# Kernel tuning notes

Measured on AMD Instinct MI355X. Metric: run time of the kernel, lower is better.

Reference implementation:

```python
import jax, jax.numpy as jnp
import numpy as np

B, N, D, H, DFF, V, L, ASTHOP = 16, 512, 256, 8, 1024, 50000, 2, 2
NEG_INF = -1e9
LRELU_SLOPE = 0.2
LN_EPS = 1e-6


def positional_encoding(length, d):
    pos = np.arange(length)[:, None].astype(np.float32)
    i = np.arange(d)[None, :].astype(np.float32)
    angle = pos / np.power(10000.0, (2.0 * np.floor(i / 2.0)) / d)
    pe = np.zeros((length, d), dtype=np.float32)
    pe[:, 0::2] = np.sin(angle[:, 0::2])
    pe[:, 1::2] = np.cos(angle[:, 1::2])
    return jnp.asarray(pe[None])  # [1, length, d]


def layer_norm(x, g, b):
    mu = jnp.mean(x, axis=-1, keepdims=True)
    var = jnp.mean((x - mu) ** 2, axis=-1, keepdims=True)
    return (x - mu) * jax.lax.rsqrt(var + LN_EPS) * g + b


def setup_inputs() -> dict:
    key = jax.random.key(0)
    ks = jax.random.split(key, 16)
    s = 0.02
    f32 = jnp.float32
    return {
        "node_input": jax.random.randint(ks[0], (B, N), 0, V, dtype=jnp.int32),
        "edge_input": jax.random.randint(ks[1], (B, N, N), 0, 2, dtype=jnp.int32),
        "mha_mask": jnp.zeros((B, 1, 1, N), jnp.int32),
        "training": 0,
        "embed": jax.random.normal(ks[2], (V, D), f32) * s,
        "Wg": jax.random.normal(ks[3], (D, D), f32) * s,
        "a1": jax.random.normal(ks[4], (D, 1), f32) * s,
        "a2": jax.random.normal(ks[5], (D, 1), f32) * s,
        "Wq": jax.random.normal(ks[6], (L, D, D), f32) * s,
        "bq": jnp.zeros((L, D), f32),
        "Wk": jax.random.normal(ks[7], (L, D, D), f32) * s,
        "bk": jnp.zeros((L, D), f32),
        "Wv": jax.random.normal(ks[8], (L, D, D), f32) * s,
        "bv": jnp.zeros((L, D), f32),
        "Wo": jax.random.normal(ks[9], (L, D, D), f32) * s,
        "bo": jnp.zeros((L, D), f32),
        "W1": jax.random.normal(ks[10], (L, D, DFF), f32) * s,
        "b1": jnp.zeros((L, DFF), f32),
        "W2": jax.random.normal(ks[11], (L, DFF, D), f32) * s,
        "b2": jnp.zeros((L, D), f32),
        "ln1_g": jnp.ones((L, D), f32),
        "ln1_b": jnp.zeros((L, D), f32),
        "ln2_g": jnp.ones((L, D), f32),
        "ln2_b": jnp.zeros((L, D), f32),
    }


def reference(node_input, edge_input, mha_mask, training, embed, Wg, a1, a2,
              Wq, bq, Wk, bk, Wv, bv, Wo, bo, W1, b1, W2, b2,
              ln1_g, ln1_b, ln2_g, ln2_b):
    del training  # inference: dropout is identity
    pe = positional_encoding(N, D)
    adj = edge_input > 0  # [B,N,N] bool

    x = embed[node_input]  # [B,N,D] embedding lookup
    # --- GAT message-passing hops (shared weights) ---
    for _ in range(ASTHOP):
        h = x @ Wg  # [B,N,D]
        # e_ij = LeakyReLU(a1.h_i + a2.h_j)
        e = jax.nn.leaky_relu(h @ a1 + jnp.swapaxes(h @ a2, 1, 2), LRELU_SLOPE)
        e = jnp.where(adj, e, NEG_INF)
        alpha = jax.nn.softmax(e, axis=-1)  # [B,N,N]
        x = jax.nn.elu(jnp.einsum('bij,bjd->bid', alpha, h))

    # --- scale + positional encoding ---
    x = x * jnp.sqrt(jnp.float32(D)) + pe[:, :N, :]

    # --- transformer encoder stack ---
    mask = mha_mask.astype(x.dtype)  # [B,1,1,N], 1 = pad
    dh = D // H
    attn = None
    for l in range(L):
        q = (x @ Wq[l] + bq[l]).reshape(B, N, H, dh).transpose(0, 2, 1, 3)
        k = (x @ Wk[l] + bk[l]).reshape(B, N, H, dh).transpose(0, 2, 1, 3)
        v = (x @ Wv[l] + bv[l]).reshape(B, N, H, dh).transpose(0, 2, 1, 3)
        scores = jnp.einsum('bhqd,bhkd->bhqk', q, k) / jnp.sqrt(jnp.float32(dh))
        scores = scores + mask * NEG_INF
        attn = jax.nn.softmax(scores, axis=-1)  # [B,H,N,N]
        o = jnp.einsum('bhqk,bhkd->bhqd', attn, v).transpose(0, 2, 1, 3).reshape(B, N, D)
        x = layer_norm(x + o @ Wo[l] + bo[l], ln1_g[l], ln1_b[l])
        f = jax.nn.relu(x @ W1[l] + b1[l]) @ W2[l] + b2[l]
        x = layer_norm(x + f, ln2_g[l], ln2_b[l])
    return (x, attn)
```

## Files before the change

kernel.cpp:

```cpp
#include <hip/hip_runtime.h>
#include <math.h>

#define B_    16
#define N_    512
#define D_    256
#define H_    8
#define DH_   32
#define DFF_  1024
#define L_    2
#define NEG_INF_ (-1e9f)
#define LRELU_ 0.2f

typedef __attribute__((ext_vector_type(8))) short bf8_t;
typedef __attribute__((ext_vector_type(8))) unsigned short us8;
typedef __attribute__((ext_vector_type(4))) float f4_t;

__device__ __forceinline__ unsigned short f2bf(float f) {
    union { float f; unsigned u; } v; v.f = f;
    unsigned r = v.u + 0x7FFF + ((v.u >> 16) & 1);
    return (unsigned short)(r >> 16);
}
__device__ __forceinline__ float bf2f(unsigned short h) {
    union { unsigned u; float f; } v; v.u = ((unsigned)h) << 16;
    return v.f;
}

__device__ __forceinline__ void gl_lds16(const void* g, void* l) {
    __builtin_amdgcn_global_load_lds(
        (const __attribute__((address_space(1))) unsigned int*)g,
        (__attribute__((address_space(3))) unsigned int*)l, 16, 0, 0);
}

template <int BM, int BN, int WROWS, int WCOLS>
__global__ __launch_bounds__(256) void mfma_gemm(
    const unsigned short* __restrict__ Ag, const unsigned short* __restrict__ Btg,
    const float* __restrict__ bias,
    float* __restrict__ Cfg, unsigned short* __restrict__ Chg, int trans,
    int K, int lda, int ldb, int ldc,
    int inner, long sAo, long sAi, long sBo, long sBi, long sCo, long sCi,
    float scale, int act)
{
    constexpr int TM = BM / WROWS, TN = BN / WCOLS;
    constexpr int MT = TM / 16, NT = TN / 16;

    int z  = blockIdx.z;
    int zo = z / inner;
    int zi = z - zo * inner;
    const unsigned short* Ab = Ag + (long)zo * sAo + (long)zi * sAi;
    const unsigned short* Bt = Btg + (long)zo * sBo + (long)zi * sBi;
    long co = (long)zo * sCo + (long)zi * sCi;

    int bm = blockIdx.y * BM;
    int bn = blockIdx.x * BN;
    int tid  = threadIdx.x;
    int lane = tid & 63;
    int w    = tid >> 6;
    int wr   = w / WCOLS, wc = w - wr * WCOLS;

    __shared__ unsigned short As[BM * 32];
    __shared__ unsigned short Bs[BN * 32];

    f4_t acc[MT][NT] = {};

    int lrow = lane & 15;
    int koff = (lane >> 4) * 8;

    for (int k0 = 0; k0 < K; k0 += 32) {
#pragma unroll
        for (int t = w; t < BM / 16; t += 4) {
            int s = t * 512 + lane * 8;
            int r = s >> 5, c = s & 31;
            gl_lds16(Ab + (long)(bm + r) * lda + k0 + c, &As[t * 512]);
        }
#pragma unroll
        for (int t = w; t < BN / 16; t += 4) {
            int s = t * 512 + lane * 8;
            int r = s >> 5, c = s & 31;
            gl_lds16(Bt + (long)(bn + r) * ldb + k0 + c, &Bs[t * 512]);
        }
        __syncthreads();

        bf8_t af[MT], bfr[NT];
#pragma unroll
        for (int mi = 0; mi < MT; mi++)
            af[mi] = *(const bf8_t*)&As[(wr * TM + mi * 16 + lrow) * 32 + koff];
#pragma unroll
        for (int ni = 0; ni < NT; ni++)
            bfr[ni] = *(const bf8_t*)&Bs[(wc * TN + ni * 16 + lrow) * 32 + koff];
#pragma unroll
        for (int mi = 0; mi < MT; mi++)
#pragma unroll
            for (int ni = 0; ni < NT; ni++)
                acc[mi][ni] = __builtin_amdgcn_mfma_f32_16x16x32_bf16(
                    af[mi], bfr[ni], acc[mi][ni], 0, 0, 0);
        __syncthreads();
    }

#pragma unroll
    for (int mi = 0; mi < MT; mi++) {
#pragma unroll
        for (int ni = 0; ni < NT; ni++) {
            int row0 = bm + wr * TM + mi * 16 + (lane >> 4) * 4;
            int col  = bn + wc * TN + ni * 16 + (lane & 15);
            float bv = bias ? bias[col] : 0.f;
            float vv[4];
#pragma unroll
            for (int r = 0; r < 4; r++) {
                float v = acc[mi][ni][r] * scale + bv;
                if (act == 1) v = fmaxf(v, 0.f);
                else if (act == 2) v = v > 0.f ? v : (__expf(v) - 1.f);
                vv[r] = v;
            }
            if (trans) {
                ushort4 u = make_ushort4(f2bf(vv[0]), f2bf(vv[1]), f2bf(vv[2]), f2bf(vv[3]));
                *(ushort4*)&Chg[co + (long)col * ldc + row0] = u;
            } else {
                if (Cfg) {
#pragma unroll
                    for (int r = 0; r < 4; r++)
                        Cfg[co + (long)(row0 + r) * ldc + col] = vv[r];
                }
                if (Chg) {
#pragma unroll
                    for (int r = 0; r < 4; r++)
                        Chg[co + (long)(row0 + r) * ldc + col] = f2bf(vv[r]);
                }
            }
        }
    }
}

template <bool WRITE_ATTN>
__global__ __launch_bounds__(256) void attn_fused(
    const unsigned short* __restrict__ QKV,
    const int* __restrict__ mask,
    float* __restrict__ attn_out,
    unsigned short* __restrict__ Ob)
{
    int bh = blockIdx.x;
    int b  = bh >> 3, h = bh & 7;
    int q0 = blockIdx.y * 64;
    int tid  = threadIdx.x;
    int lane = tid & 63, w = tid >> 6;
    int lrow = lane & 15, quad = lane >> 4;

    __shared__ unsigned short Ks[512 * 40];
    __shared__ unsigned short Vs[32 * 136];
    __shared__ float maskf[512];
    unsigned short* Ps = Ks;

    const long tokbase = (long)b * N_;

#pragma unroll
    for (int i = 0; i < 8; i++) {
        int idx = tid + i * 256;
        int row = idx >> 2, seg = idx & 3;
        us8 v = *(const us8*)&QKV[(tokbase + row) * 768 + 256 + h * 32 + seg * 8];
        *(us8*)&Ks[row * 40 + seg * 8] = v;
    }
    maskf[tid]       = (float)mask[b * N_ + tid] * NEG_INF_;
    maskf[tid + 256] = (float)mask[b * N_ + tid + 256] * NEG_INF_;

    bf8_t aq = *(const bf8_t*)&QKV[(tokbase + q0 + w * 16 + lrow) * 768 + h * 32 + quad * 8];
    __syncthreads();

    f4_t acc[32];
    f4_t zero = {0.f, 0.f, 0.f, 0.f};
#pragma unroll
    for (int ni = 0; ni < 32; ni++) {
        bf8_t bk = *(const bf8_t*)&Ks[(ni * 16 + lrow) * 40 + quad * 8];
        acc[ni] = __builtin_amdgcn_mfma_f32_16x16x32_bf16(aq, bk, zero, 0, 0, 0);
    }

    const float rscale = 0.17677669529663687f;
    float mr[4] = {-3e38f, -3e38f, -3e38f, -3e38f};
#pragma unroll
    for (int ni = 0; ni < 32; ni++) {
        float mk = maskf[ni * 16 + lrow];
#pragma unroll
        for (int r = 0; r < 4; r++) {
            float v = acc[ni][r] * rscale + mk;
            acc[ni][r] = v;
            mr[r] = fmaxf(mr[r], v);
        }
    }
#pragma unroll
    for (int r = 0; r < 4; r++) {
        mr[r] = fmaxf(mr[r], __shfl_xor(mr[r], 1));
        mr[r] = fmaxf(mr[r], __shfl_xor(mr[r], 2));
        mr[r] = fmaxf(mr[r], __shfl_xor(mr[r], 4));
        mr[r] = fmaxf(mr[r], __shfl_xor(mr[r], 8));
    }
    float sr[4] = {0.f, 0.f, 0.f, 0.f};
#pragma unroll
    for (int ni = 0; ni < 32; ni++) {
#pragma unroll
        for (int r = 0; r < 4; r++) {
            float p = __expf(acc[ni][r] - mr[r]);
            acc[ni][r] = p;
            sr[r] += p;
        }
    }
#pragma unroll
    for (int r = 0; r < 4; r++) {
        sr[r] += __shfl_xor(sr[r], 1);
        sr[r] += __shfl_xor(sr[r], 2);
        sr[r] += __shfl_xor(sr[r], 4);
        sr[r] += __shfl_xor(sr[r], 8);
        sr[r] = 1.f / sr[r];
    }
#pragma unroll
    for (int ni = 0; ni < 32; ni++)
#pragma unroll
        for (int r = 0; r < 4; r++)
            acc[ni][r] *= sr[r];

    if (WRITE_ATTN) {
#pragma unroll
        for (int ni = 0; ni < 32; ni++) {
#pragma unroll
            for (int r = 0; r < 4; r++)
                attn_out[((long)bh * N_ + q0 + w * 16 + quad * 4 + r) * N_ + ni * 16 + lrow]
                    = acc[ni][r];
        }
    }

    f4_t oacc[2] = {{0.f,0.f,0.f,0.f}, {0.f,0.f,0.f,0.f}};
    for (int c = 0; c < 4; c++) {
        __syncthreads();
        {
            int kk = tid >> 1, dseg = (tid & 1) * 16;
            const unsigned short* src =
                &QKV[(tokbase + c * 128 + kk) * 768 + 512 + h * 32 + dseg];
            us8 v0 = *(const us8*)src;
            us8 v1 = *(const us8*)(src + 8);
#pragma unroll
            for (int jj = 0; jj < 8; jj++) {
                Vs[(dseg + jj) * 136 + kk]     = v0[jj];
                Vs[(dseg + 8 + jj) * 136 + kk] = v1[jj];
            }
        }
#pragma unroll
        for (int ni = 0; ni < 8; ni++) {
            int nn = c * 8 + ni;
#pragma unroll
            for (int r = 0; r < 4; r++)
                Ps[w * 2176 + (quad * 4 + r) * 136 + ni * 16 + lrow] = f2bf(acc[nn][r]);
        }
        __syncthreads();
#pragma unroll
        for (int k8 = 0; k8 < 4; k8++) {
            bf8_t ap = *(const bf8_t*)&Ps[w * 2176 + lrow * 136 + k8 * 32 + quad * 8];
#pragma unroll
            for (int t = 0; t < 2; t++) {
                bf8_t bvf = *(const bf8_t*)&Vs[(t * 16 + lrow) * 136 + k8 * 32 + quad * 8];
                oacc[t] = __builtin_amdgcn_mfma_f32_16x16x32_bf16(ap, bvf, oacc[t], 0, 0, 0);
            }
        }
    }

#pragma unroll
    for (int t = 0; t < 2; t++)
#pragma unroll
        for (int r = 0; r < 4; r++)
            Ob[(tokbase + q0 + w * 16 + quad * 4 + r) * 256 + h * 32 + t * 16 + lrow]
                = f2bf(oacc[t][r]);
}

struct ConvJobs {
    const float* src[13];
    unsigned short* dst[13];
    int R[13];
    int C[13];
};

__global__ __launch_bounds__(256) void conv_transpose(ConvJobs j)
{
    int z = blockIdx.z;
    int R = j.R[z], C = j.C[z];
    int r0 = blockIdx.y * 64, c0 = blockIdx.x * 64;
    if (r0 >= R || c0 >= C) return;
    __shared__ float t[64][65];
    const float* src = j.src[z];
    unsigned short* dst = j.dst[z];
    int tx = threadIdx.x & 63, ty = threadIdx.x >> 6;
#pragma unroll
    for (int i = 0; i < 16; i++) {
        int r = ty + i * 4;
        t[r][tx] = src[(long)(r0 + r) * C + c0 + tx];
    }
    __syncthreads();
#pragma unroll
    for (int i = 0; i < 16; i++) {
        int c = ty + i * 4;
        dst[(long)(c0 + c) * R + r0 + tx] = f2bf(t[tx][c]);
    }
}

__global__ __launch_bounds__(256) void pack_bias(const float* __restrict__ bq,
                                                 const float* __restrict__ bk,
                                                 const float* __restrict__ bv,
                                                 float* __restrict__ bc)
{
    int i = blockIdx.x * 256 + threadIdx.x;
    int l = i / 768, c = i - l * 768;
    float v = (c < 256) ? bq[l * 256 + c]
            : (c < 512) ? bk[l * 256 + c - 256]
                        : bv[l * 256 + c - 512];
    bc[i] = v;
}

__global__ __launch_bounds__(64) void gather_embed(const int* __restrict__ idx,
                                                   const float* __restrict__ embed,
                                                   float* __restrict__ X,
                                                   unsigned short* __restrict__ Xb)
{
    int row = blockIdx.x;
    int id  = idx[row];
    float4 v = ((const float4*)(embed + (long)id * D_))[threadIdx.x];
    ((float4*)(X + (long)row * D_))[threadIdx.x] = v;
    ((ushort4*)(Xb + (long)row * D_))[threadIdx.x] =
        make_ushort4(f2bf(v.x), f2bf(v.y), f2bf(v.z), f2bf(v.w));
}

__global__ __launch_bounds__(256) void gat_s12T(const unsigned short* __restrict__ hT,
                                                const float* __restrict__ a1,
                                                const float* __restrict__ a2,
                                                float* __restrict__ s1,
                                                float* __restrict__ s2)
{
    int j = blockIdx.x * 256 + threadIdx.x;
    float d1 = 0.f, d2 = 0.f;
    for (int d = 0; d < D_; d++) {
        float hv = bf2f(hT[(long)d * (B_ * N_) + j]);
        d1 += hv * a1[d];
        d2 += hv * a2[d];
    }
    s1[j] = d1;
    s2[j] = d2;
}

__global__ __launch_bounds__(256) void gat_alpha(const float* __restrict__ s1,
                                                 const float* __restrict__ s2,
                                                 const int* __restrict__ edges,
                                                 unsigned short* __restrict__ alpha)
{
    int row = blockIdx.x;
    int b   = row >> 9;
    const int*   erow = edges + (long)row * N_;
    const float* s2b  = s2 + (long)b * N_;
    float si = s1[row];
    int t = threadIdx.x;

    float e  = si + s2b[t];
    e = e > 0.f ? e : LRELU_ * e;
    float v0 = (erow[t] > 0) ? e : NEG_INF_;
    float e2 = si + s2b[t + 256];
    e2 = e2 > 0.f ? e2 : LRELU_ * e2;
    float v1 = (erow[t + 256] > 0) ? e2 : NEG_INF_;

    __shared__ float redm[4], reds[4];
    float m = fmaxf(v0, v1);
    for (int off = 32; off; off >>= 1) m = fmaxf(m, __shfl_xor(m, off));
    if ((t & 63) == 0) redm[t >> 6] = m;
    __syncthreads();
    m = fmaxf(fmaxf(redm[0], redm[1]), fmaxf(redm[2], redm[3]));
    float x0 = __expf(v0 - m), x1 = __expf(v1 - m);
    float s = x0 + x1;
    for (int off = 32; off; off >>= 1) s += __shfl_xor(s, off);
    if ((t & 63) == 0) reds[t >> 6] = s;
    __syncthreads();
    s = reds[0] + reds[1] + reds[2] + reds[3];
    float inv = 1.f / s;
    alpha[(long)row * N_ + t]       = f2bf(x0 * inv);
    alpha[(long)row * N_ + t + 256] = f2bf(x1 * inv);
}

__global__ __launch_bounds__(64) void ln_add(const float* __restrict__ x,
                                             const float* __restrict__ tm,
                                             const float* __restrict__ g,
                                             const float* __restrict__ bta,
                                             float* __restrict__ out,
                                             unsigned short* __restrict__ outb)
{
    long row  = blockIdx.x;
    int  lane = threadIdx.x;
    float4 xv = ((const float4*)(x + row * D_))[lane];
    float4 tv = ((const float4*)(tm + row * D_))[lane];
    float4 v = make_float4(xv.x + tv.x, xv.y + tv.y, xv.z + tv.z, xv.w + tv.w);
    float s = v.x + v.y + v.z + v.w;
    for (int off = 32; off; off >>= 1) s += __shfl_xor(s, off);
    float mean = s * (1.f / D_);
    float4 d = make_float4(v.x - mean, v.y - mean, v.z - mean, v.w - mean);
    float sq = d.x * d.x + d.y * d.y + d.z * d.z + d.w * d.w;
    for (int off = 32; off; off >>= 1) sq += __shfl_xor(sq, off);
    float rs = rsqrtf(sq * (1.f / D_) + 1e-6f);
    float4 gv = ((const float4*)g)[lane];
    float4 bv = ((const float4*)bta)[lane];
    float4 o = make_float4(d.x * rs * gv.x + bv.x, d.y * rs * gv.y + bv.y,
                           d.z * rs * gv.z + bv.z, d.w * rs * gv.w + bv.w);
    ((float4*)(out + row * D_))[lane] = o;
    ((ushort4*)(outb + row * D_))[lane] =
        make_ushort4(f2bf(o.x), f2bf(o.y), f2bf(o.z), f2bf(o.w));
}

__global__ __launch_bounds__(256) void scale_pe(float* __restrict__ X,
                                                unsigned short* __restrict__ Xb)
{
    int row = blockIdx.x;
    int n = row & (N_ - 1);
    int d = threadIdx.x;
    float expo = (float)(d & ~1) * (1.0f / D_);
    float inv  = powf(10000.0f, -expo);
    float ang  = (float)n * inv;
    float pe   = (d & 1) ? cosf(ang) : sinf(ang);
    long idx = (long)row * D_ + d;
    float v = X[idx] * 16.0f + pe;
    X[idx]  = v;
    Xb[idx] = f2bf(v);
}

__global__ __launch_bounds__(256) void copy_f4(const float4* __restrict__ src,
                                               float4* __restrict__ dst, long n4)
{
    long i = (long)blockIdx.x * 256 + threadIdx.x;
    if (i < n4) dst[i] = src[i];
}

extern "C" void kernel_launch(void* const* d_in, const int* in_sizes, int n_in,
                              void* d_out, int out_size, void* d_ws, size_t ws_size,
                              hipStream_t stream)
{
    const int*   node  = (const int*)d_in[0];
    const int*   edge  = (const int*)d_in[1];
    const int*   mask  = (const int*)d_in[2];
    const float* embed = (const float*)d_in[4];
    const float* Wg    = (const float*)d_in[5];
    const float* a1    = (const float*)d_in[6];
    const float* a2    = (const float*)d_in[7];
    const float* Wq    = (const float*)d_in[8];
    const float* bq    = (const float*)d_in[9];
    const float* Wk    = (const float*)d_in[10];
    const float* bk    = (const float*)d_in[11];
    const float* Wv    = (const float*)d_in[12];
    const float* bv    = (const float*)d_in[13];
    const float* Wo    = (const float*)d_in[14];
    const float* bo    = (const float*)d_in[15];
    const float* W1    = (const float*)d_in[16];
    const float* b1    = (const float*)d_in[17];
    const float* W2    = (const float*)d_in[18];
    const float* b2    = (const float*)d_in[19];
    const float* ln1g  = (const float*)d_in[20];
    const float* ln1b  = (const float*)d_in[21];
    const float* ln2g  = (const float*)d_in[22];
    const float* ln2b  = (const float*)d_in[23];

    const long XSZ = (long)B_ * N_ * D_;
    const int  MR  = B_ * N_;
    float* outx = (float*)d_out;
    float* ATT  = outx + XSZ;

    float*          X    = (float*)d_ws;
    unsigned short* Xb   = (unsigned short*)(X + XSZ);
    float*          Hb   = (float*)(Xb + XSZ);
    unsigned short* alphab = (unsigned short*)Hb;
    unsigned short* QKVb = (unsigned short*)(Hb + XSZ);
    unsigned short* hT   = QKVb;
    unsigned short* Ob   = QKVb + (long)MR * 768;
    unsigned short* Fb   = Ob + XSZ;
    float* S1 = (float*)(Fb + (long)MR * DFF_);
    float* S2 = S1 + MR;
    unsigned short* WgT = (unsigned short*)(S2 + MR);
    unsigned short* Wc  = WgT + 65536;
    unsigned short* WoT = Wc + 2 * 768 * 256;
    unsigned short* W1T = WoT + 2 * 65536;
    unsigned short* W2T = W1T + 2 * 262144;
    float*          bc  = (float*)(W2T + 2 * 262144);

    ConvJobs j;
    j.src[0] = Wg;  j.dst[0] = WgT;  j.R[0] = 256;  j.C[0] = 256;
    for (int l = 0; l < 2; l++) {
        j.src[1 + l] = Wq + l * 65536;  j.dst[1 + l] = Wc + l * 196608;           j.R[1+l] = 256;  j.C[1+l] = 256;
        j.src[3 + l] = Wk + l * 65536;  j.dst[3 + l] = Wc + l * 196608 + 65536;   j.R[3+l] = 256;  j.C[3+l] = 256;
        j.src[5 + l] = Wv + l * 65536;  j.dst[5 + l] = Wc + l * 196608 + 131072;  j.R[5+l] = 256;  j.C[5+l] = 256;
        j.src[7 + l] = Wo + l * 65536;  j.dst[7 + l] = WoT + l * 65536;           j.R[7+l] = 256;  j.C[7+l] = 256;
        j.src[9 + l] = W1 + l * 262144; j.dst[9 + l] = W1T + l * 262144;          j.R[9+l] = 256;  j.C[9+l] = 1024;
        j.src[11+ l] = W2 + l * 262144; j.dst[11+ l] = W2T + l * 262144;          j.R[11+l]= 1024; j.C[11+l]= 256;
    }
    conv_transpose<<<dim3(16, 16, 13), 256, 0, stream>>>(j);
    pack_bias<<<6, 256, 0, stream>>>(bq, bk, bv, bc);

    gather_embed<<<MR, 64, 0, stream>>>(node, embed, X, Xb);

    for (int hop = 0; hop < 2; hop++) {
        mfma_gemm<128,128,2,2><<<dim3(2, 64, 1), 256, 0, stream>>>(
            Xb, WgT, nullptr, nullptr, hT, 1,
            256, 256, 256, MR, 1, 0,0, 0,0, 0,0, 1.f, 0);
        gat_s12T<<<32, 256, 0, stream>>>(hT, a1, a2, S1, S2);
        gat_alpha<<<MR, 256, 0, stream>>>(S1, S2, edge, alphab);
        mfma_gemm<128,128,2,2><<<dim3(2, 4, 16), 256, 0, stream>>>(
            alphab, hT, nullptr, X, Xb, 0,
            512, 512, MR, 256, 1,
            (long)N_*N_, 0, (long)N_, 0, (long)N_*D_, 0, 1.f, 2);
    }

    scale_pe<<<MR, 256, 0, stream>>>(X, Xb);

    for (int l = 0; l < L_; l++) {
        mfma_gemm<128,128,2,2><<<dim3(6, 64, 1), 256, 0, stream>>>(
            Xb, Wc + l * 196608, bc + l * 768, nullptr, QKVb, 0,
            256, 256, 256, 768, 1, 0,0, 0,0, 0,0, 1.f, 0);

        if (l == L_ - 1)
            attn_fused<true><<<dim3(128, 8, 1), 256, 0, stream>>>(QKVb, mask, ATT, Ob);
        else
            attn_fused<false><<<dim3(128, 8, 1), 256, 0, stream>>>(QKVb, mask, nullptr, Ob);

        mfma_gemm<128,128,2,2><<<dim3(2, 64, 1), 256, 0, stream>>>(
            Ob, WoT + l * 65536, bo + l * D_, Hb, nullptr, 0,
            256, 256, 256, 256, 1, 0,0, 0,0, 0,0, 1.f, 0);
        ln_add<<<MR, 64, 0, stream>>>(X, Hb, ln1g + l * D_, ln1b + l * D_, X, Xb);

        mfma_gemm<128,128,2,2><<<dim3(8, 64, 1), 256, 0, stream>>>(
            Xb, W1T + l * 262144, b1 + l * DFF_, nullptr, Fb, 0,
            256, 256, 256, 1024, 1, 0,0, 0,0, 0,0, 1.f, 1);
        mfma_gemm<128,128,2,2><<<dim3(2, 64, 1), 256, 0, stream>>>(
            Fb, W2T + l * 262144, b2 + l * D_, Hb, nullptr, 0,
            1024, 1024, 1024, 256, 1, 0,0, 0,0, 0,0, 1.f, 0);
        ln_add<<<MR, 64, 0, stream>>>(X, Hb, ln2g + l * D_, ln2b + l * D_, X, Xb);
    }

    long n4 = XSZ / 4;
    copy_f4<<<(unsigned)((n4 + 255) / 256), 256, 0, stream>>>((const float4*)X,
                                                              (float4*)outx, n4);
}
```

Before: 597.8 us.

## Double-buffer GEMM LDS tiles, split GAT score reduction, fuse final copy into layernorm

The MFMA GEMM now uses two LDS buffers and issues the next K-slice load before computing on the current one, so global-to-LDS traffic can overlap with MFMA work. The GAT score kernel splits the 256-wide dot product across four wave groups and sums the partials through shared memory, launching four times as many blocks for more parallelism. The last layernorm writes straight to the output buffer, which removes the separate copy kernel and the unused bf16 store. The positional encoding replaces powf with __expf, which changes numerics slightly, and the extra LDS buffer doubles shared memory use per GEMM block.

```diff
diff --git a/kernel.cpp b/kernel.cpp
--- a/kernel.cpp
+++ b/kernel.cpp
@@ -57,36 +57,44 @@
     int w    = tid >> 6;
     int wr   = w / WCOLS, wc = w - wr * WCOLS;
 
-    __shared__ unsigned short As[BM * 32];
-    __shared__ unsigned short Bs[BN * 32];
+    __shared__ unsigned short As[2][BM * 32];
+    __shared__ unsigned short Bs[2][BN * 32];
 
     f4_t acc[MT][NT] = {};
 
     int lrow = lane & 15;
     int koff = (lane >> 4) * 8;
 
-    for (int k0 = 0; k0 < K; k0 += 32) {
+    auto stage = [&](int buf, int k0) {
 #pragma unroll
         for (int t = w; t < BM / 16; t += 4) {
             int s = t * 512 + lane * 8;
             int r = s >> 5, c = s & 31;
-            gl_lds16(Ab + (long)(bm + r) * lda + k0 + c, &As[t * 512]);
+            gl_lds16(Ab + (long)(bm + r) * lda + k0 + c, &As[buf][t * 512]);
         }
 #pragma unroll
         for (int t = w; t < BN / 16; t += 4) {
             int s = t * 512 + lane * 8;
             int r = s >> 5, c = s & 31;
-            gl_lds16(Bt + (long)(bn + r) * ldb + k0 + c, &Bs[t * 512]);
-        }
-        __syncthreads();
+            gl_lds16(Bt + (long)(bn + r) * ldb + k0 + c, &Bs[buf][t * 512]);
+        }
+    };
+
+    int nk = K >> 5;
+    stage(0, 0);
+    __syncthreads();
+
+    for (int t = 0; t < nk; t++) {
+        int cur = t & 1;
+        if (t + 1 < nk) stage(cur ^ 1, (t + 1) << 5);
 
         bf8_t af[MT], bfr[NT];
 #pragma unroll
         for (int mi = 0; mi < MT; mi++)
-            af[mi] = *(const bf8_t*)&As[(wr * TM + mi * 16 + lrow) * 32 + koff];
+            af[mi] = *(const bf8_t*)&As[cur][(wr * TM + mi * 16 + lrow) * 32 + koff];
 #pragma unroll
         for (int ni = 0; ni < NT; ni++)
-            bfr[ni] = *(const bf8_t*)&Bs[(wc * TN + ni * 16 + lrow) * 32 + koff];
+            bfr[ni] = *(const bf8_t*)&Bs[cur][(wc * TN + ni * 16 + lrow) * 32 + koff];
 #pragma unroll
         for (int mi = 0; mi < MT; mi++)
 #pragma unroll
@@ -329,15 +337,24 @@
                                                 float* __restrict__ s1,
                                                 float* __restrict__ s2)
 {
-    int j = blockIdx.x * 256 + threadIdx.x;
+    int lane = threadIdx.x & 63;
+    int dq   = threadIdx.x >> 6;
+    int j = blockIdx.x * 64 + lane;
     float d1 = 0.f, d2 = 0.f;
-    for (int d = 0; d < D_; d++) {
+#pragma unroll 8
+    for (int d = dq * 64; d < dq * 64 + 64; d++) {
         float hv = bf2f(hT[(long)d * (B_ * N_) + j]);
         d1 += hv * a1[d];
         d2 += hv * a2[d];
     }
-    s1[j] = d1;
-    s2[j] = d2;
+    __shared__ float r1[4][64], r2[4][64];
+    r1[dq][lane] = d1;
+    r2[dq][lane] = d2;
+    __syncthreads();
+    if (dq == 0) {
+        s1[j] = r1[0][lane] + r1[1][lane] + r1[2][lane] + r1[3][lane];
+        s2[j] = r2[0][lane] + r2[1][lane] + r2[2][lane] + r2[3][lane];
+    }
 }
 
 __global__ __launch_bounds__(256) void gat_alpha(const float* __restrict__ s1,
@@ -400,8 +417,9 @@
     float4 o = make_float4(d.x * rs * gv.x + bv.x, d.y * rs * gv.y + bv.y,
                            d.z * rs * gv.z + bv.z, d.w * rs * gv.w + bv.w);
     ((float4*)(out + row * D_))[lane] = o;
-    ((ushort4*)(outb + row * D_))[lane] =
-        make_ushort4(f2bf(o.x), f2bf(o.y), f2bf(o.z), f2bf(o.w));
+    if (outb)
+        ((ushort4*)(outb + row * D_))[lane] =
+            make_ushort4(f2bf(o.x), f2bf(o.y), f2bf(o.z), f2bf(o.w));
 }
 
 __global__ __launch_bounds__(256) void scale_pe(float* __restrict__ X,
@@ -411,20 +429,13 @@
     int n = row & (N_ - 1);
     int d = threadIdx.x;
     float expo = (float)(d & ~1) * (1.0f / D_);
-    float inv  = powf(10000.0f, -expo);
+    float inv  = __expf(-expo * 9.210340371976184f);
     float ang  = (float)n * inv;
     float pe   = (d & 1) ? cosf(ang) : sinf(ang);
     long idx = (long)row * D_ + d;
     float v = X[idx] * 16.0f + pe;
     X[idx]  = v;
     Xb[idx] = f2bf(v);
-}
-
-__global__ __launch_bounds__(256) void copy_f4(const float4* __restrict__ src,
-                                               float4* __restrict__ dst, long n4)
-{
-    long i = (long)blockIdx.x * 256 + threadIdx.x;
-    if (i < n4) dst[i] = src[i];
 }
 
 extern "C" void kernel_launch(void* const* d_in, const int* in_sizes, int n_in,
@@ -496,7 +507,7 @@
         mfma_gemm<128,128,2,2><<<dim3(2, 64, 1), 256, 0, stream>>>(
             Xb, WgT, nullptr, nullptr, hT, 1,
             256, 256, 256, MR, 1, 0,0, 0,0, 0,0, 1.f, 0);
-        gat_s12T<<<32, 256, 0, stream>>>(hT, a1, a2, S1, S2);
+        gat_s12T<<<128, 256, 0, stream>>>(hT, a1, a2, S1, S2);
         gat_alpha<<<MR, 256, 0, stream>>>(S1, S2, edge, alphab);
         mfma_gemm<128,128,2,2><<<dim3(2, 4, 16), 256, 0, stream>>>(
             alphab, hT, nullptr, X, Xb, 0,
@@ -527,10 +538,9 @@
         mfma_gemm<128,128,2,2><<<dim3(2, 64, 1), 256, 0, stream>>>(
             Fb, W2T + l * 262144, b2 + l * D_, Hb, nullptr, 0,
             1024, 1024, 1024, 256, 1, 0,0, 0,0, 0,0, 1.f, 0);
-        ln_add<<<MR, 64, 0, stream>>>(X, Hb, ln2g + l * D_, ln2b + l * D_, X, Xb);
-    }
-
-    long n4 = XSZ / 4;
-    copy_f4<<<(unsigned)((n4 + 255) / 256), 256, 0, stream>>>((const float4*)X,
-                                                              (float4*)outx, n4);
-}
+        if (l == L_ - 1)
+            ln_add<<<MR, 64, 0, stream>>>(X, Hb, ln2g + l * D_, ln2b + l * D_, outx, nullptr);
+        else
+            ln_add<<<MR, 64, 0, stream>>>(X, Hb, ln2g + l * D_, ln2b + l * D_, X, Xb);
+    }
+}
```

Result: faster. 573.2 us (-4.1%).
